# Kernel optimization log

Hardware: AMD Instinct MI355X
Metric: run time of the kernel (lower is better)

The kernel has to match this reference:

```python
import jax, jax.numpy as jnp
import numpy as np

N_NODES = 100_000
N_EDGES = 1_600_000
N_GRAPHS = 512
NF = 64        # n_node_feats
H1 = 128       # hidden width
H2 = 64        # dim_node_emb
DIM_OUT = 1
STEPS = 4      # set2set processing steps


def _lin(x, W, b):
    # torch Linear convention: y = x @ W.T + b, W: [out, in]
    return x @ W.T + b


def _gelu(x):
    return jax.nn.gelu(x, approximate=False)  # torch.nn.GELU default (erf)


def _lstm_cell(x, h, c, Wih, Whh, bih, bhh):
    g = x @ Wih.T + bih + h @ Whh.T + bhh
    i, f, gg, o = jnp.split(g, 4, axis=-1)  # torch gate order: i, f, g, o
    i, f, o = jax.nn.sigmoid(i), jax.nn.sigmoid(f), jax.nn.sigmoid(o)
    gg = jnp.tanh(gg)
    c = f * c + i * gg
    h = o * jnp.tanh(c)
    return h, c


def setup_inputs() -> dict:
    key = jax.random.key(0)
    ks = jax.random.split(key, 24)
    p = lambda k, shp: jax.random.normal(k, shp, dtype=jnp.float32) * 0.05
    inp = {
        "x": jax.random.normal(ks[0], (N_NODES, NF), dtype=jnp.float32),
        "edge_index": jax.random.randint(ks[1], (2, N_EDGES), 0, N_NODES, dtype=jnp.int32),
        "batch": jnp.sort(jax.random.randint(ks[2], (N_NODES,), 0, N_GRAPHS, dtype=jnp.int32)),
        "nfc_W": p(ks[3], (H1, NF)), "nfc_b": p(ks[4], (H1,)),
        "gc1_W": p(ks[5], (H1, H1)), "gc1_b": p(ks[6], (H1,)),
        "gc2_W": p(ks[7], (H2, H1)), "gc2_b": p(ks[8], (H2,)),
        "lstm0_Wih": p(ks[9], (4 * H2, 2 * H2)), "lstm0_Whh": p(ks[10], (4 * H2, H2)),
        "lstm0_bih": p(ks[11], (4 * H2,)), "lstm0_bhh": p(ks[12], (4 * H2,)),
        "lstm1_Wih": p(ks[13], (4 * H2, H2)), "lstm1_Whh": p(ks[14], (4 * H2, H2)),
        "lstm1_bih": p(ks[15], (4 * H2,)), "lstm1_bhh": p(ks[16], (4 * H2,)),
        "fc1_W": p(ks[17], (32, 2 * H2)), "fc1_b": p(ks[18], (32,)),
        "fc2_W": p(ks[19], (DIM_OUT, 32)), "fc2_b": p(ks[20], (DIM_OUT,)),
    }
    return inp


def _forward(x, edge_index, batch, nfc_W, nfc_b, gc1_W, gc1_b, gc2_W, gc2_b,
             lstm0_Wih, lstm0_Whh, lstm0_bih, lstm0_bhh,
             lstm1_Wih, lstm1_Whh, lstm1_bih, lstm1_bhh,
             fc1_W, fc1_b, fc2_W, fc2_b):
    src, dst = edge_index[0], edge_index[1]

    def gin_conv(h, W, b):
        # PyG GINConv, eps=0: lin((1+eps)*x + sum_{j in N(i)} x_j)
        agg = jax.ops.segment_sum(h[src], dst, num_segments=N_NODES)
        return _lin(h + agg, W, b)

    h = _gelu(_lin(x, nfc_W, nfc_b))
    h = _gelu(gin_conv(h, gc1_W, gc1_b))
    h = _gelu(gin_conv(h, gc2_W, gc2_b))
    # F.normalize(p=2, dim=1)
    h = h / jnp.maximum(jnp.linalg.norm(h, axis=1, keepdims=True), 1e-12)

    # Set2Set: 2-layer LSTM, 4 processing steps, scatter-softmax attention
    B = N_GRAPHS
    h0 = jnp.zeros((B, H2), jnp.float32); c0 = jnp.zeros((B, H2), jnp.float32)
    h1 = jnp.zeros((B, H2), jnp.float32); c1 = jnp.zeros((B, H2), jnp.float32)
    q_star = jnp.zeros((B, 2 * H2), jnp.float32)
    for _ in range(STEPS):
        h0, c0 = _lstm_cell(q_star, h0, c0, lstm0_Wih, lstm0_Whh, lstm0_bih, lstm0_bhh)
        h1, c1 = _lstm_cell(h0, h1, c1, lstm1_Wih, lstm1_Whh, lstm1_bih, lstm1_bhh)
        q = h1  # [B, H2]
        e = jnp.sum(h * q[batch], axis=-1, keepdims=True)  # [N, 1]
        m = jax.ops.segment_max(e, batch, num_segments=B)
        ex = jnp.exp(e - m[batch])
        s = jax.ops.segment_sum(ex, batch, num_segments=B)
        a = ex / (s[batch] + 1e-16)
        r = jax.ops.segment_sum(a * h, batch, num_segments=B)  # [B, H2]
        q_star = jnp.concatenate([q, r], axis=-1)

    z = _gelu(_lin(q_star, fc1_W, fc1_b))
    z = _lin(z, fc2_W, fc2_b)
    return z, h


def reference(x, edge_index, batch, nfc_W, nfc_b, gc1_W, gc1_b, gc2_W, gc2_b,
              lstm0_Wih, lstm0_Whh, lstm0_bih, lstm0_bhh,
              lstm1_Wih, lstm1_Whh, lstm1_bih, lstm1_bhh,
              fc1_W, fc1_b, fc2_W, fc2_b):
    return _forward(x, edge_index, batch, nfc_W, nfc_b, gc1_W, gc1_b, gc2_W, gc2_b,
                    lstm0_Wih, lstm0_Whh, lstm0_bih, lstm0_bhh,
                    lstm1_Wih, lstm1_Whh, lstm1_bih, lstm1_bhh,
                    fc1_W, fc1_b, fc2_W, fc2_b)
```

## Files before the change

kernel.cpp:

```cpp
#include <hip/hip_runtime.h>
#include <hip/hip_bf16.h>
#include <hip/hip_fp16.h>
#include <math.h>

constexpr int N  = 100000;
constexpr int E  = 1600000;
constexpr int NG = 512;
constexpr int NF = 64;
constexpr int H1 = 128;
constexpr int H2 = 64;

constexpr int BW   = 128;
constexpr int NB   = (N + BW - 1) / BW;
constexpr int CAP  = 2600;
constexpr int CHUNK = 4096;

constexpr int MAXN = 416;
constexpr int RST  = 68;

typedef __attribute__((ext_vector_type(8))) short short8;
typedef __attribute__((ext_vector_type(4))) float f32x4;

__device__ __forceinline__ float gelu_f(float x) {
    return 0.5f * x * (1.0f + erff(x * 0.70710678118654752f));
}
__device__ __forceinline__ float sigmoid_f(float x) {
    return 1.0f / (1.0f + expf(-x));
}
__device__ __forceinline__ float waveAllSum(float v) {
    #pragma unroll
    for (int m = 32; m; m >>= 1) v += __shfl_xor(v, m);
    return v;
}
__device__ __forceinline__ unsigned short f2bf(float x) {
    __hip_bfloat16 b = __float2bfloat16(x);
    return *reinterpret_cast<unsigned short*>(&b);
}
__device__ __forceinline__ float bf2f(unsigned short u) {
    return __uint_as_float(((unsigned int)u) << 16);
}
__device__ __forceinline__ float bf_lo(unsigned int u) { return __uint_as_float(u << 16); }
__device__ __forceinline__ float bf_hi(unsigned int u) { return __uint_as_float(u & 0xffff0000u); }

__device__ __forceinline__ void bfsplit(float v, unsigned short& hi, unsigned short& lo) {
    hi = f2bf(v);
    lo = f2bf(v - bf2f(hi));
}

__device__ __forceinline__ void pack8(float4 a, float4 b, short8& h8, short8& l8) {
    unsigned short h0,h1,h2,h3,h4,h5,h6,h7,l0,l1,l2,l3,l4,l5,l6,l7;
    bfsplit(a.x,h0,l0); bfsplit(a.y,h1,l1); bfsplit(a.z,h2,l2); bfsplit(a.w,h3,l3);
    bfsplit(b.x,h4,l4); bfsplit(b.y,h5,l5); bfsplit(b.z,h6,l6); bfsplit(b.w,h7,l7);
    union { uint4 u; short8 s; } th, tl;
    th.u = make_uint4((unsigned)h0|((unsigned)h1<<16),(unsigned)h2|((unsigned)h3<<16),
                      (unsigned)h4|((unsigned)h5<<16),(unsigned)h6|((unsigned)h7<<16));
    tl.u = make_uint4((unsigned)l0|((unsigned)l1<<16),(unsigned)l2|((unsigned)l3<<16),
                      (unsigned)l4|((unsigned)l5<<16),(unsigned)l6|((unsigned)l7<<16));
    h8 = th.s; l8 = tl.s;
}

__global__ __launch_bounds__(256) void setup_kernel(const int* __restrict__ batch,
                                                    const float* __restrict__ Wih0, const float* __restrict__ Whh0,
                                                    const float* __restrict__ bih0, const float* __restrict__ bhh0,
                                                    const float* __restrict__ Wih1, const float* __restrict__ Whh1,
                                                    const float* __restrict__ bih1, const float* __restrict__ bhh1,
                                                    const float* __restrict__ gc1W, const float* __restrict__ gc2W,
                                                    const float* __restrict__ nfcW,
                                                    float* __restrict__ WT0, float* __restrict__ WT1,
                                                    float* __restrict__ b0, float* __restrict__ b1,
                                                    unsigned short* __restrict__ W1F, unsigned short* __restrict__ W2F,
                                                    unsigned short* __restrict__ W0F,
                                                    int* __restrict__ bcursor, int* __restrict__ gstart) {
    int i = blockIdx.x * 256 + threadIdx.x;
    if (i < 192 * 256) {
        int k = i >> 8, j = i & 255;
        WT0[i] = (k < 128) ? Wih0[j * 128 + k] : Whh0[j * 64 + (k - 128)];
    }
    if (i < 128 * 256) {
        int k = i >> 8, j = i & 255;
        WT1[i] = (k < 64) ? Wih1[j * 64 + k] : Whh1[j * 64 + (k - 64)];
    }
    if (i < 16384) {
        int f = i >> 9, r = i & 511, l = r >> 3, j = r & 7;
        int c = f >> 3, ct = f & 7;
        int o = ct * 16 + (l & 15), k = c * 32 + (l >> 4) * 8 + j;
        unsigned short hi, lo;
        bfsplit(gc1W[o * 128 + k], hi, lo);
        W1F[f * 1024 + r] = hi;
        W1F[f * 1024 + 512 + r] = lo;
    }
    if (i < 8192) {
        int f = i >> 9, r = i & 511, l = r >> 3, j = r & 7;
        int c2 = f >> 2, ct2 = f & 3;
        int o = ct2 * 16 + (l & 15), k = c2 * 32 + (l >> 4) * 8 + j;
        unsigned short hi, lo;
        bfsplit(gc2W[o * 128 + k], hi, lo);
        W2F[f * 1024 + r] = hi;
        W2F[f * 1024 + 512 + r] = lo;
    }
    if (i < 8192) {
        int f = i >> 9, r = i & 511, l = r >> 3, j = r & 7;
        int c = f >> 3, ct = f & 7;
        int o = ct * 16 + (l & 15), k = c * 32 + (l >> 4) * 8 + j;
        unsigned short hi, lo;
        bfsplit(nfcW[o * 64 + k], hi, lo);
        W0F[f * 1024 + r] = hi;
        W0F[f * 1024 + 512 + r] = lo;
    }
    if (i < 256) { b0[i] = bih0[i] + bhh0[i]; b1[i] = bih1[i] + bhh1[i]; }
    if (i < NB) bcursor[i] = i * CAP;
    if (i <= NG) {
        if (i == NG) gstart[NG] = N;
        else {
            int lo = 0, hi = N;
            while (lo < hi) {
                int mid = (lo + hi) >> 1;
                if (batch[mid] < i) lo = mid + 1; else hi = mid;
            }
            gstart[i] = lo;
        }
    }
}

__global__ __launch_bounds__(256) void bin_scatter_kernel(const int* __restrict__ ei,
                                                          int* __restrict__ bcursor,
                                                          int* __restrict__ pairs) {
    __shared__ int hist[NB];
    __shared__ int start_s[NB];
    __shared__ int lcur[NB];
    int tid = threadIdx.x;
    int e0 = blockIdx.x * CHUNK;
    for (int b = tid; b < NB; b += 256) hist[b] = 0;
    __syncthreads();
    #pragma unroll 4
    for (int k = 0; k < CHUNK / 256; ++k) {
        int e = e0 + k * 256 + tid;
        if (e < E) atomicAdd(&hist[ei[E + e] >> 7], 1);
    }
    __syncthreads();
    for (int b = tid; b < NB; b += 256) {
        if (hist[b]) start_s[b] = atomicAdd(&bcursor[b], hist[b]);
        lcur[b] = 0;
    }
    __syncthreads();
    #pragma unroll 4
    for (int k = 0; k < CHUNK / 256; ++k) {
        int e = e0 + k * 256 + tid;
        if (e < E) {
            int d = ei[E + e];
            int s = ei[e];
            int b = d >> 7;
            int pos = start_s[b] + atomicAdd(&lcur[b], 1);
            if (pos < (b + 1) * CAP) pairs[pos] = (s << 7) | (d & 127);
        }
    }
}

__global__ __launch_bounds__(256) void csr_bucket_kernel(const int* __restrict__ pairs,
                                                         const int* __restrict__ bcursor,
                                                         int* __restrict__ srcs,
                                                         int2* __restrict__ nrange) {
    __shared__ int cnt_l[BW];
    __shared__ int cur_l[BW];
    __shared__ int wt[2];
    int b = blockIdx.x;
    int tid = threadIdx.x;
    int base = b * CAP;
    int cnt = bcursor[b] - base;
    if (cnt > CAP) cnt = CAP;
    if (tid < BW) cnt_l[tid] = 0;
    __syncthreads();
    for (int i = tid; i < cnt; i += 256) {
        atomicAdd(&cnt_l[pairs[base + i] & 127], 1);
    }
    __syncthreads();
    if (tid < BW) {
        int v = cnt_l[tid];
        int lane = tid & 63, w = tid >> 6;
        int incl = v;
        #pragma unroll
        for (int off = 1; off < 64; off <<= 1) {
            int t = __shfl_up(incl, off);
            if (lane >= off) incl += t;
        }
        if (lane == 63) wt[w] = incl;
        __syncthreads();
        int excl = (w ? wt[0] : 0) + incl - v;
        int node = b * BW + tid;
        if (node < N) nrange[node] = make_int2(base + excl, base + excl + v);
        cur_l[tid] = excl;
    } else {
        __syncthreads();
    }
    __syncthreads();
    for (int i = tid; i < cnt; i += 256) {
        int p = pairs[base + i];
        int pos = atomicAdd(&cur_l[p & 127], 1);
        srcs[base + pos] = p >> 7;
    }
}

__global__ __launch_bounds__(512, 2) void lin1_kernel(const float* __restrict__ x,
                                                      const uint4* __restrict__ W0F,
                                                      const float* __restrict__ bias,
                                                      unsigned short* __restrict__ out_bf, int nrows) {
    constexpr int EPS = 136;
    __shared__ __align__(16) uint4 w0lds[2048];
    __shared__ __align__(16) unsigned short eps[8][16 * EPS];
    union U8 { uint4 u; short8 s; };
    int tid = threadIdx.x, w = tid >> 6, lane = tid & 63;
    int m15 = lane & 15, quad = lane >> 4;
    int rowbase = blockIdx.x * 128 + w * 16;
    int r0 = rowbase + m15; if (r0 >= nrows) r0 = nrows - 1;

    #pragma unroll
    for (int i = 0; i < 4; ++i) w0lds[i * 512 + tid] = W0F[i * 512 + tid];
    __syncthreads();

    f32x4 acc[8];
    #pragma unroll
    for (int ct = 0; ct < 8; ++ct) acc[ct] = (f32x4)0.f;

    float4 p0[2][2];
    #pragma unroll
    for (int c = 0; c < 2; ++c) {
        p0[c][0] = *(const float4*)&x[(size_t)r0 * 64 + c * 32 + quad * 8];
        p0[c][1] = *(const float4*)&x[(size_t)r0 * 64 + c * 32 + quad * 8 + 4];
    }

    #pragma unroll
    for (int c = 0; c < 2; ++c) {
        short8 ah0, al0;
        pack8(p0[c][0], p0[c][1], ah0, al0);
        #pragma unroll
        for (int ct = 0; ct < 8; ++ct) {
            U8 th, tl;
            th.u = w0lds[(c * 8 + ct) * 128 + lane];
            tl.u = w0lds[(c * 8 + ct) * 128 + 64 + lane];
            short8 bh = th.s, bl = tl.s;
            acc[ct] = __builtin_amdgcn_mfma_f32_16x16x32_bf16(ah0, bh, acc[ct], 0, 0, 0);
            acc[ct] = __builtin_amdgcn_mfma_f32_16x16x32_bf16(ah0, bl, acc[ct], 0, 0, 0);
            acc[ct] = __builtin_amdgcn_mfma_f32_16x16x32_bf16(al0, bh, acc[ct], 0, 0, 0);
        }
    }

    unsigned short* ep = eps[w];
    #pragma unroll
    for (int ct = 0; ct < 8; ++ct) {
        float bc = bias[ct * 16 + m15];
        #pragma unroll
        for (int r = 0; r < 4; ++r) {
            int node = quad * 4 + r;
            ep[node * EPS + ct * 16 + m15] = f2bf(gelu_f(acc[ct][r] + bc));
        }
    }
    asm volatile("s_waitcnt lgkmcnt(0)" ::: "memory");
    #pragma unroll
    for (int it = 0; it < 4; ++it) {
        int idx = it * 64 + lane;
        int rowl = idx >> 4, off = (idx & 15) * 8;
        int grow = rowbase + rowl;
        if (grow < nrows)
            *(uint4*)(out_bf + (size_t)grow * 128 + off) = *(const uint4*)&ep[rowl * EPS + off];
    }
}

__global__ __launch_bounds__(256) void agg_kernel(const uint4* __restrict__ h4,
                                                  const int2* __restrict__ nrange,
                                                  const int* __restrict__ srcs,
                                                  uint4* __restrict__ utab) {
    int wave = threadIdx.x >> 6, lane = threadIdx.x & 63;
    int qw = lane >> 4, ql = lane & 15;
    int n = blockIdx.x * 4 + wave;
    if (n >= N) return;
    int2 rng = nrange[n];
    int s0 = rng.x, deg = rng.y - rng.x;
    int m1 = deg < 64 ? deg : 64;
    int pre = (lane < m1) ? srcs[s0 + lane] : 0;
    float a0 = 0.f, a1 = 0.f, a2 = 0.f, a3 = 0.f, a4 = 0.f, a5 = 0.f, a6 = 0.f, a7 = 0.f;
    auto addu = [&](uint4 u) {
        a0 += bf_lo(u.x); a1 += bf_hi(u.x); a2 += bf_lo(u.y); a3 += bf_hi(u.y);
        a4 += bf_lo(u.z); a5 += bf_hi(u.z); a6 += bf_lo(u.w); a7 += bf_hi(u.w);
    };
    int t = 0;
    for (; t + 16 <= m1; t += 16) {
        int i0 = __shfl(pre, t + qw);
        int i1 = __shfl(pre, t + 4 + qw);
        int i2 = __shfl(pre, t + 8 + qw);
        int i3 = __shfl(pre, t + 12 + qw);
        uint4 u0 = h4[(size_t)i0 * 16 + ql];
        uint4 u1 = h4[(size_t)i1 * 16 + ql];
        uint4 u2 = h4[(size_t)i2 * 16 + ql];
        uint4 u3 = h4[(size_t)i3 * 16 + ql];
        addu(u0); addu(u1); addu(u2); addu(u3);
    }
    for (; t < m1; t += 4) {
        int idx = t + qw;
        int s = __shfl(pre, idx < m1 ? idx : 0);
        if (idx < m1) addu(h4[(size_t)s * 16 + ql]);
    }
    for (int j = 64 + qw; j < deg; j += 4) addu(h4[(size_t)srcs[s0 + j] * 16 + ql]);
    a0 += __shfl_down(a0, 32); a1 += __shfl_down(a1, 32);
    a2 += __shfl_down(a2, 32); a3 += __shfl_down(a3, 32);
    a4 += __shfl_down(a4, 32); a5 += __shfl_down(a5, 32);
    a6 += __shfl_down(a6, 32); a7 += __shfl_down(a7, 32);
    a0 += __shfl_down(a0, 16); a1 += __shfl_down(a1, 16);
    a2 += __shfl_down(a2, 16); a3 += __shfl_down(a3, 16);
    a4 += __shfl_down(a4, 16); a5 += __shfl_down(a5, 16);
    a6 += __shfl_down(a6, 16); a7 += __shfl_down(a7, 16);
    if (qw == 0) {
        addu(h4[(size_t)n * 16 + ql]);
        unsigned short h0, h1, h2, h3, h4_, h5, h6, h7;
        unsigned short l0, l1, l2, l3, l4, l5, l6, l7;
        bfsplit(a0, h0, l0); bfsplit(a1, h1, l1);
        bfsplit(a2, h2, l2); bfsplit(a3, h3, l3);
        bfsplit(a4, h4_, l4); bfsplit(a5, h5, l5);
        bfsplit(a6, h6, l6); bfsplit(a7, h7, l7);
        uint4 o0, o1;
        o0.x = (unsigned)h0 | ((unsigned)h1 << 16);
        o0.y = (unsigned)h2 | ((unsigned)h3 << 16);
        o0.z = (unsigned)l0 | ((unsigned)l1 << 16);
        o0.w = (unsigned)l2 | ((unsigned)l3 << 16);
        o1.x = (unsigned)h4_ | ((unsigned)h5 << 16);
        o1.y = (unsigned)h6 | ((unsigned)h7 << 16);
        o1.z = (unsigned)l4 | ((unsigned)l5 << 16);
        o1.w = (unsigned)l6 | ((unsigned)l7 << 16);
        utab[(size_t)n * 32 + 2 * ql]     = o0;
        utab[(size_t)n * 32 + 2 * ql + 1] = o1;
    }
}

__global__ __launch_bounds__(512, 2) void lin2_fused_kernel(const uint4* __restrict__ in4,
                                                            const uint4* __restrict__ W1F,
                                                            const float* __restrict__ b1,
                                                            const uint4* __restrict__ W2F,
                                                            unsigned short* __restrict__ y2,
                                                            int nrows) {
    constexpr int AST2 = 40;
    __shared__ __align__(16) uint4 wlds[6144];
    __shared__ __align__(16) unsigned short relds[8 * 1280];
    union U8 { uint4 u; short8 s; };
    int tid = threadIdx.x, w = tid >> 6, lane = tid & 63;
    int m15 = lane & 15, quad = lane >> 4;
    unsigned short* myL = relds + w * 1280;
    int rowbase = blockIdx.x * 128 + w * 16;
    int r0 = rowbase + m15; if (r0 >= nrows) r0 = nrows - 1;
    const uint4* a0p = in4 + (size_t)r0 * 32 + quad * 2;

    #pragma unroll
    for (int i = 0; i < 12; ++i) {
        int idx = i * 512 + tid;
        wlds[idx] = (idx < 4096) ? W1F[idx] : W2F[idx - 4096];
    }

    uint4 a[8];
    #pragma unroll
    for (int c = 0; c < 4; ++c) { a[2 * c] = a0p[c * 8]; a[2 * c + 1] = a0p[c * 8 + 1]; }

    float bc[8];
    #pragma unroll
    for (int ct = 0; ct < 8; ++ct) bc[ct] = b1[ct * 16 + m15];

    __syncthreads();
    const uint4* W1L = wlds;
    const uint4* W2L = wlds + 4096;

    f32x4 acc[8];
    #pragma unroll
    for (int ct = 0; ct < 8; ++ct) acc[ct] = (f32x4)0.f;

    #pragma unroll
    for (int c = 0; c < 4; ++c) {
        U8 t;
        uint4 u00 = a[2 * c], u01 = a[2 * c + 1];
        t.u = make_uint4(u00.x, u00.y, u01.x, u01.y); short8 ah0 = t.s;
        t.u = make_uint4(u00.z, u00.w, u01.z, u01.w); short8 al0 = t.s;
        #pragma unroll
        for (int ct = 0; ct < 8; ++ct) {
            U8 th, tl;
            th.u = W1L[(c * 8 + ct) * 128 + lane];
            tl.u = W1L[(c * 8 + ct) * 128 + 64 + lane];
            short8 bh = th.s, bl = tl.s;
            acc[ct] = __builtin_amdgcn_mfma_f32_16x16x32_bf16(ah0, bh, acc[ct], 0, 0, 0);
            acc[ct] = __builtin_amdgcn_mfma_f32_16x16x32_bf16(ah0, bl, acc[ct], 0, 0, 0);
            acc[ct] = __builtin_amdgcn_mfma_f32_16x16x32_bf16(al0, bh, acc[ct], 0, 0, 0);
        }
    }

    #pragma unroll
    for (int ct = 0; ct < 8; ++ct)
        #pragma unroll
        for (int r = 0; r < 4; ++r)
            acc[ct][r] = gelu_f(acc[ct][r] + bc[ct]);

    unsigned short* Ahi2 = myL;
    unsigned short* Alo2 = myL + 16 * AST2;
    f32x4 acc2[4];
    #pragma unroll
    for (int ct = 0; ct < 4; ++ct) acc2[ct] = (f32x4)0.f;

    #pragma unroll
    for (int c2 = 0; c2 < 4; ++c2) {
        #pragma unroll
        for (int cc = 0; cc < 2; ++cc) {
            int ct = c2 * 2 + cc;
            #pragma unroll
            for (int r = 0; r < 4; ++r) {
                int node = quad * 4 + r;
                unsigned short hi, lo;
                bfsplit(acc[ct][r], hi, lo);
                Ahi2[node * AST2 + cc * 16 + m15] = hi;
                Alo2[node * AST2 + cc * 16 + m15] = lo;
            }
        }
        asm volatile("s_waitcnt lgkmcnt(0)" ::: "memory");
        short8 ah0 = *(const short8*)&Ahi2[m15 * AST2 + quad * 8];
        short8 al0 = *(const short8*)&Alo2[m15 * AST2 + quad * 8];
        #pragma unroll
        for (int ct2 = 0; ct2 < 4; ++ct2) {
            U8 th, tl;
            th.u = W2L[(c2 * 4 + ct2) * 128 + lane];
            tl.u = W2L[(c2 * 4 + ct2) * 128 + 64 + lane];
            short8 bh = th.s, bl = tl.s;
            acc2[ct2] = __builtin_amdgcn_mfma_f32_16x16x32_bf16(ah0, bh, acc2[ct2], 0, 0, 0);
            acc2[ct2] = __builtin_amdgcn_mfma_f32_16x16x32_bf16(ah0, bl, acc2[ct2], 0, 0, 0);
            acc2[ct2] = __builtin_amdgcn_mfma_f32_16x16x32_bf16(al0, bh, acc2[ct2], 0, 0, 0);
        }
    }

    unsigned short* ep = myL;
    #pragma unroll
    for (int ct2 = 0; ct2 < 4; ++ct2)
        #pragma unroll
        for (int r = 0; r < 4; ++r) {
            int node = quad * 4 + r;
            __half hv = __float2half(acc2[ct2][r]);
            ep[node * 72 + ct2 * 16 + m15] = *reinterpret_cast<unsigned short*>(&hv);
        }
    asm volatile("s_waitcnt lgkmcnt(0)" ::: "memory");
    #pragma unroll
    for (int it = 0; it < 2; ++it) {
        int idx = it * 64 + lane;
        int rowl = idx >> 3, off = (idx & 7) * 8;
        int grow = rowbase + rowl;
        if (grow < nrows)
            *(uint4*)(y2 + (size_t)grow * 64 + off) = *(const uint4*)&ep[rowl * 72 + off];
    }
}

__global__ __launch_bounds__(256) void agg2_norm_kernel(const uint2* __restrict__ y2,
                                                        const int2* __restrict__ nrange,
                                                        const int* __restrict__ srcs,
                                                        const float* __restrict__ b2,
                                                        float* __restrict__ hn) {
    int wave = threadIdx.x >> 6, lane = threadIdx.x & 63;
    int qw = lane >> 4, ql = lane & 15;
    int n = blockIdx.x * 4 + wave;
    if (n >= N) return;
    int2 rng = nrange[n];
    int s0 = rng.x, deg = rng.y - rng.x;
    int m1 = deg < 64 ? deg : 64;
    int pre = (lane < m1) ? srcs[s0 + lane] : 0;
    float a0 = 0.f, a1 = 0.f, a2 = 0.f, a3 = 0.f;
    auto addu = [&](uint2 u) {
        float2 f01 = __half22float2(*reinterpret_cast<__half2*>(&u.x));
        float2 f23 = __half22float2(*reinterpret_cast<__half2*>(&u.y));
        a0 += f01.x; a1 += f01.y; a2 += f23.x; a3 += f23.y;
    };
    int t = 0;
    for (; t + 16 <= m1; t += 16) {
        int i0 = __shfl(pre, t + qw);
        int i1 = __shfl(pre, t + 4 + qw);
        int i2 = __shfl(pre, t + 8 + qw);
        int i3 = __shfl(pre, t + 12 + qw);
        uint2 u0 = y2[(size_t)i0 * 16 + ql];
        uint2 u1 = y2[(size_t)i1 * 16 + ql];
        uint2 u2 = y2[(size_t)i2 * 16 + ql];
        uint2 u3 = y2[(size_t)i3 * 16 + ql];
        addu(u0); addu(u1); addu(u2); addu(u3);
    }
    for (; t < m1; t += 4) {
        int idx = t + qw;
        int s = __shfl(pre, idx < m1 ? idx : 0);
        if (idx < m1) addu(y2[(size_t)s * 16 + ql]);
    }
    for (int j = 64 + qw; j < deg; j += 4) addu(y2[(size_t)srcs[s0 + j] * 16 + ql]);
    a0 += __shfl_down(a0, 32); a1 += __shfl_down(a1, 32);
    a2 += __shfl_down(a2, 32); a3 += __shfl_down(a3, 32);
    a0 += __shfl_down(a0, 16); a1 += __shfl_down(a1, 16);
    a2 += __shfl_down(a2, 16); a3 += __shfl_down(a3, 16);
    if (qw == 0) {
        addu(y2[(size_t)n * 16 + ql]);
        float4 bv = *(const float4*)&b2[ql * 4];
        float v0 = gelu_f(a0 + bv.x), v1 = gelu_f(a1 + bv.y);
        float v2 = gelu_f(a2 + bv.z), v3 = gelu_f(a3 + bv.w);
        float ss = v0 * v0 + v1 * v1 + v2 * v2 + v3 * v3;
        #pragma unroll
        for (int mm = 1; mm < 16; mm <<= 1) ss += __shfl_xor(ss, mm);
        float d = fmaxf(sqrtf(ss), 1e-12f);
        *(float4*)&hn[(size_t)n * 64 + ql * 4] = make_float4(v0 / d, v1 / d, v2 / d, v3 / d);
    }
}

__global__ __launch_bounds__(256) void set2set_kernel(const float* __restrict__ hn,
                                                      const int* __restrict__ gstart,
                                                      const float* __restrict__ WT0, const float* __restrict__ b0,
                                                      const float* __restrict__ WT1, const float* __restrict__ b1,
                                                      float* __restrict__ qstar_out) {
    __shared__ __align__(16) unsigned short hL[MAXN * RST];
    __shared__ float av[MAXN];
    __shared__ __align__(16) float xc0[192];
    __shared__ __align__(16) float xc1[128];
    __shared__ __align__(16) float gates[256];
    __shared__ float c0v[H2], c1v[H2];
    __shared__ float red[4];
    __shared__ float rp[4][H2];
    __shared__ float sp[4];

    int g = blockIdx.x;
    int tid = threadIdx.x, w = tid >> 6, lane = tid & 63;
    int s0 = gstart[g], s1 = gstart[g + 1];
    int cnt = s1 - s0;
    int cL = cnt < MAXN ? cnt : MAXN;
    const float* hq = xc1 + 64;

    for (int idx = tid; idx < cL * 16; idx += 256) {
        int n = idx >> 4, p4 = idx & 15;
        float4 v = *(const float4*)&hn[(size_t)(s0 + n) * 64 + p4 * 4];
        uint2 u;
        u.x = (unsigned int)f2bf(v.x) | ((unsigned int)f2bf(v.y) << 16);
        u.y = (unsigned int)f2bf(v.z) | ((unsigned int)f2bf(v.w) << 16);
        *(uint2*)&hL[n * RST + p4 * 4] = u;
    }
    if (tid < 192) xc0[tid] = 0.f;
    if (tid < 128) xc1[tid] = 0.f;
    if (tid < H2) { c0v[tid] = 0.f; c1v[tid] = 0.f; }
    float b0v = b0[tid], b1v = b1[tid];
    __syncthreads();

    for (int step = 0; step < 4; ++step) {
        {
            float a0 = 0.f, a1 = 0.f, a2 = 0.f, a3 = 0.f;
            #pragma unroll 8
            for (int k = 0; k < 192; k += 4) {
                a0 += xc0[k]     * WT0[(k)     * 256 + tid];
                a1 += xc0[k + 1] * WT0[(k + 1) * 256 + tid];
                a2 += xc0[k + 2] * WT0[(k + 2) * 256 + tid];
                a3 += xc0[k + 3] * WT0[(k + 3) * 256 + tid];
            }
            gates[tid] = (a0 + a1) + (a2 + a3) + b0v;
        }
        __syncthreads();
        if (tid < H2) {
            float ii = sigmoid_f(gates[tid]), ff = sigmoid_f(gates[H2 + tid]);
            float gg = tanhf(gates[2 * H2 + tid]), oo = sigmoid_f(gates[3 * H2 + tid]);
            float c = ff * c0v[tid] + ii * gg;
            float h = oo * tanhf(c);
            c0v[tid] = c; xc0[128 + tid] = h; xc1[tid] = h;
        }
        __syncthreads();
        {
            float a0 = 0.f, a1 = 0.f, a2 = 0.f, a3 = 0.f;
            #pragma unroll 8
            for (int k = 0; k < 128; k += 4) {
                a0 += xc1[k]     * WT1[(k)     * 256 + tid];
                a1 += xc1[k + 1] * WT1[(k + 1) * 256 + tid];
                a2 += xc1[k + 2] * WT1[(k + 2) * 256 + tid];
                a3 += xc1[k + 3] * WT1[(k + 3) * 256 + tid];
            }
            gates[tid] = (a0 + a1) + (a2 + a3) + b1v;
        }
        __syncthreads();
        if (tid < H2) {
            float ii = sigmoid_f(gates[tid]), ff = sigmoid_f(gates[H2 + tid]);
            float gg = tanhf(gates[2 * H2 + tid]), oo = sigmoid_f(gates[3 * H2 + tid]);
            float c = ff * c1v[tid] + ii * gg;
            float h = oo * tanhf(c);
            c1v[tid] = c; xc1[64 + tid] = h;
        }
        __syncthreads();

        float lm = -INFINITY;
        for (int i = tid; i < cnt; i += 256) {
            float e = 0.f;
            if (i < MAXN) {
                const uint2* row = (const uint2*)&hL[i * RST];
                #pragma unroll
                for (int p4 = 0; p4 < 16; ++p4) {
                    uint2 u = row[p4];
                    e += bf_lo(u.x) * hq[p4 * 4 + 0];
                    e += bf_hi(u.x) * hq[p4 * 4 + 1];
                    e += bf_lo(u.y) * hq[p4 * 4 + 2];
                    e += bf_hi(u.y) * hq[p4 * 4 + 3];
                }
                av[i] = e;
            } else {
                for (int f = 0; f < 64; ++f) e += hn[(size_t)(s0 + i) * 64 + f] * hq[f];
            }
            lm = fmaxf(lm, e);
        }
        #pragma unroll
        for (int mm = 32; mm; mm >>= 1) lm = fmaxf(lm, __shfl_xor(lm, mm));
        if (lane == 0) red[w] = lm;
        __syncthreads();
        float m = fmaxf(fmaxf(red[0], red[1]), fmaxf(red[2], red[3]));

        float ps = 0.f;
        for (int i = tid; i < cnt; i += 256) {
            float e;
            if (i < MAXN) e = av[i];
            else {
                e = 0.f;
                for (int f = 0; f < 64; ++f) e += hn[(size_t)(s0 + i) * 64 + f] * hq[f];
            }
            float p = expf(e - m);
            ps += p;
            if (i < MAXN) av[i] = p;
        }
        ps = waveAllSum(ps);
        if (lane == 0) sp[w] = ps;
        __syncthreads();
        float s = sp[0] + sp[1] + sp[2] + sp[3];

        float racc = 0.f;
        for (int i = w; i < cL; i += 4) {
            unsigned short hv = hL[i * RST + lane];
            racc += av[i] * bf2f(hv);
        }
        float qf = hq[lane];
        for (int n = MAXN + w; n < cnt; n += 4) {
            float v = hn[(size_t)(s0 + n) * 64 + lane];
            float e = waveAllSum(v * qf);
            float p = expf(e - m);
            racc += p * v;
        }
        rp[w][lane] = racc;
        __syncthreads();
        if (tid < H2) {
            float r = 0.f;
            if (cnt > 0) {
                r = (rp[0][tid] + rp[1][tid] + rp[2][tid] + rp[3][tid]) / (s + 1e-16f);
            }
            xc0[tid] = xc1[64 + tid];
            xc0[H2 + tid] = r;
        }
        __syncthreads();
    }
    if (tid < 2 * H2) qstar_out[g * 2 * H2 + tid] = xc0[tid];
}

__global__ __launch_bounds__(256) void fcout_kernel(const float* __restrict__ q_star,
                                                    const float* __restrict__ W1, const float* __restrict__ b1,
                                                    const float* __restrict__ W2, const float* __restrict__ b2,
                                                    float* __restrict__ z) {
    __shared__ float W1l[32 * 128];
    __shared__ float b1l[32], W2l[32];
    int tid = threadIdx.x;
    for (int i = tid; i < 32 * 128; i += 256) W1l[i] = W1[i];
    if (tid < 32) { b1l[tid] = b1[tid]; W2l[tid] = W2[tid]; }
    __syncthreads();
    int g = blockIdx.x * 256 + tid;
    float acc[32];
    #pragma unroll
    for (int j = 0; j < 32; ++j) acc[j] = b1l[j];
    for (int k = 0; k < 128; ++k) {
        float qv = q_star[g * 128 + k];
        #pragma unroll
        for (int j = 0; j < 32; ++j) acc[j] += qv * W1l[j * 128 + k];
    }
    float zv = b2[0];
    #pragma unroll
    for (int j = 0; j < 32; ++j) zv += gelu_f(acc[j]) * W2l[j];
    z[g] = zv;
}

extern "C" void kernel_launch(void* const* d_in, const int* in_sizes, int n_in,
                              void* d_out, int out_size, void* d_ws, size_t ws_size,
                              hipStream_t stream) {
    const float* x       = (const float*)d_in[0];
    const int*   ei      = (const int*)d_in[1];
    const int*   batch   = (const int*)d_in[2];
    const float* nfc_W   = (const float*)d_in[3];
    const float* nfc_b   = (const float*)d_in[4];
    const float* gc1_W   = (const float*)d_in[5];
    const float* gc1_b   = (const float*)d_in[6];
    const float* gc2_W   = (const float*)d_in[7];
    const float* gc2_b   = (const float*)d_in[8];
    const float* l0_Wih  = (const float*)d_in[9];
    const float* l0_Whh  = (const float*)d_in[10];
    const float* l0_bih  = (const float*)d_in[11];
    const float* l0_bhh  = (const float*)d_in[12];
    const float* l1_Wih  = (const float*)d_in[13];
    const float* l1_Whh  = (const float*)d_in[14];
    const float* l1_bih  = (const float*)d_in[15];
    const float* l1_bhh  = (const float*)d_in[16];
    const float* fc1_W   = (const float*)d_in[17];
    const float* fc1_b   = (const float*)d_in[18];
    const float* fc2_W   = (const float*)d_in[19];
    const float* fc2_b   = (const float*)d_in[20];

    float* out = (float*)d_out;
    float* hn_out = out + NG;

    char* p = (char*)d_ws;
    auto take = [&](size_t bytes) {
        char* r = p;
        p += (bytes + 255) & ~size_t(255);
        return r;
    };
    float*          sbuf  = (float*)take((size_t)N * H1 * 4);
    unsigned short* hbbuf = (unsigned short*)take((size_t)N * H1 * 2);
    int*   srcs   = (int*)take((size_t)NB * CAP * 4);
    int2*  nrange = (int2*)take((size_t)N * 8);
    int*   bcursor= (int*)take((size_t)NB * 4);
    int*   gstart = (int*)take((size_t)(NG + 1) * 4);
    float* qstar  = (float*)take((size_t)NG * 2 * H2 * 4);
    float* WT0    = (float*)take((size_t)192 * 256 * 4);
    float* WT1    = (float*)take((size_t)128 * 256 * 4);
    float* b0     = (float*)take((size_t)256 * 4);
    float* b1     = (float*)take((size_t)256 * 4);
    unsigned short* W1F = (unsigned short*)take((size_t)32 * 1024 * 2);
    unsigned short* W2F = (unsigned short*)take((size_t)16 * 1024 * 2);
    unsigned short* W0F = (unsigned short*)take((size_t)16 * 1024 * 2);

    int* pairs = (int*)sbuf;

    setup_kernel<<<192, 256, 0, stream>>>(batch, l0_Wih, l0_Whh, l0_bih, l0_bhh,
                                          l1_Wih, l1_Whh, l1_bih, l1_bhh,
                                          gc1_W, gc2_W, nfc_W,
                                          WT0, WT1, b0, b1, W1F, W2F, W0F, bcursor, gstart);

    bin_scatter_kernel<<<(E + CHUNK - 1) / CHUNK, 256, 0, stream>>>(ei, bcursor, pairs);
    csr_bucket_kernel<<<NB, 256, 0, stream>>>(pairs, bcursor, srcs, nrange);

    int linGrid = (N + 127) / 128;
    lin1_kernel<<<linGrid, 512, 0, stream>>>(x, (const uint4*)W0F, nfc_b, hbbuf, N);
    agg_kernel<<<(N + 3) / 4, 256, 0, stream>>>((const uint4*)hbbuf, nrange, srcs, (uint4*)sbuf);
    lin2_fused_kernel<<<linGrid, 512, 0, stream>>>((const uint4*)sbuf, (const uint4*)W1F, gc1_b,
                                                   (const uint4*)W2F, hbbuf, N);
    agg2_norm_kernel<<<(N + 3) / 4, 256, 0, stream>>>((const uint2*)hbbuf, nrange, srcs,
                                                      gc2_b, hn_out);

    set2set_kernel<<<NG, 256, 0, stream>>>(hn_out, gstart, WT0, b0, WT1, b1, qstar);

    fcout_kernel<<<2, 256, 0, stream>>>(qstar, fc1_W, fc1_b, fc2_W, fc2_b, out);
}
```

Measured before the change: 408.7 us.

## Split first aggregation into feature halves and fuse output MLP into set2set

The first neighbor aggregation now runs as two launches, each gathering only half of the 128 bf16 features per node, with 8 edges processed per wave iteration instead of 4. This shrinks each pass's gather working set so more of it stays in cache, at the cost of reading the index lists twice and adding a launch. Separately, the final fc1/GELU/fc2 head is folded into the end of the set2set kernel using a transposed fc1 weight copy in shared memory. That removes the q_star buffer round-trip and one launch, but every graph block now reloads the fc1 weights.

```diff
diff --git a/kernel.cpp b/kernel.cpp
--- a/kernel.cpp
+++ b/kernel.cpp
@@ -265,18 +265,20 @@
     }
 }
 
-__global__ __launch_bounds__(256) void agg_kernel(const uint4* __restrict__ h4,
-                                                  const int2* __restrict__ nrange,
-                                                  const int* __restrict__ srcs,
-                                                  uint4* __restrict__ utab) {
+__global__ __launch_bounds__(256) void agg_half_kernel(const uint4* __restrict__ h4,
+                                                       const int2* __restrict__ nrange,
+                                                       const int* __restrict__ srcs,
+                                                       uint4* __restrict__ utab,
+                                                       int half) {
     int wave = threadIdx.x >> 6, lane = threadIdx.x & 63;
-    int qw = lane >> 4, ql = lane & 15;
+    int ew = lane >> 3, el = lane & 7;
     int n = blockIdx.x * 4 + wave;
     if (n >= N) return;
     int2 rng = nrange[n];
     int s0 = rng.x, deg = rng.y - rng.x;
     int m1 = deg < 64 ? deg : 64;
     int pre = (lane < m1) ? srcs[s0 + lane] : 0;
+    int hofs = half * 8 + el;
     float a0 = 0.f, a1 = 0.f, a2 = 0.f, a3 = 0.f, a4 = 0.f, a5 = 0.f, a6 = 0.f, a7 = 0.f;
     auto addu = [&](uint4 u) {
         a0 += bf_lo(u.x); a1 += bf_hi(u.x); a2 += bf_lo(u.y); a3 += bf_hi(u.y);
@@ -284,22 +286,18 @@
     };
     int t = 0;
     for (; t + 16 <= m1; t += 16) {
-        int i0 = __shfl(pre, t + qw);
-        int i1 = __shfl(pre, t + 4 + qw);
-        int i2 = __shfl(pre, t + 8 + qw);
-        int i3 = __shfl(pre, t + 12 + qw);
-        uint4 u0 = h4[(size_t)i0 * 16 + ql];
-        uint4 u1 = h4[(size_t)i1 * 16 + ql];
-        uint4 u2 = h4[(size_t)i2 * 16 + ql];
-        uint4 u3 = h4[(size_t)i3 * 16 + ql];
-        addu(u0); addu(u1); addu(u2); addu(u3);
-    }
-    for (; t < m1; t += 4) {
-        int idx = t + qw;
+        int i0 = __shfl(pre, t + ew);
+        int i1 = __shfl(pre, t + 8 + ew);
+        uint4 u0 = h4[(size_t)i0 * 16 + hofs];
+        uint4 u1 = h4[(size_t)i1 * 16 + hofs];
+        addu(u0); addu(u1);
+    }
+    for (; t < m1; t += 8) {
+        int idx = t + ew;
         int s = __shfl(pre, idx < m1 ? idx : 0);
-        if (idx < m1) addu(h4[(size_t)s * 16 + ql]);
-    }
-    for (int j = 64 + qw; j < deg; j += 4) addu(h4[(size_t)srcs[s0 + j] * 16 + ql]);
+        if (idx < m1) addu(h4[(size_t)s * 16 + hofs]);
+    }
+    for (int j = 64 + ew; j < deg; j += 8) addu(h4[(size_t)srcs[s0 + j] * 16 + hofs]);
     a0 += __shfl_down(a0, 32); a1 += __shfl_down(a1, 32);
     a2 += __shfl_down(a2, 32); a3 += __shfl_down(a3, 32);
     a4 += __shfl_down(a4, 32); a5 += __shfl_down(a5, 32);
@@ -308,8 +306,12 @@
     a2 += __shfl_down(a2, 16); a3 += __shfl_down(a3, 16);
     a4 += __shfl_down(a4, 16); a5 += __shfl_down(a5, 16);
     a6 += __shfl_down(a6, 16); a7 += __shfl_down(a7, 16);
-    if (qw == 0) {
-        addu(h4[(size_t)n * 16 + ql]);
+    a0 += __shfl_down(a0, 8);  a1 += __shfl_down(a1, 8);
+    a2 += __shfl_down(a2, 8);  a3 += __shfl_down(a3, 8);
+    a4 += __shfl_down(a4, 8);  a5 += __shfl_down(a5, 8);
+    a6 += __shfl_down(a6, 8);  a7 += __shfl_down(a7, 8);
+    if (ew == 0) {
+        addu(h4[(size_t)n * 16 + hofs]);
         unsigned short h0, h1, h2, h3, h4_, h5, h6, h7;
         unsigned short l0, l1, l2, l3, l4, l5, l6, l7;
         bfsplit(a0, h0, l0); bfsplit(a1, h1, l1);
@@ -325,8 +327,9 @@
         o1.y = (unsigned)h6 | ((unsigned)h7 << 16);
         o1.z = (unsigned)l4 | ((unsigned)l5 << 16);
         o1.w = (unsigned)l6 | ((unsigned)l7 << 16);
-        utab[(size_t)n * 32 + 2 * ql]     = o0;
-        utab[(size_t)n * 32 + 2 * ql + 1] = o1;
+        int g0 = half * 16 + 2 * el;
+        utab[(size_t)n * 32 + g0]     = o0;
+        utab[(size_t)n * 32 + g0 + 1] = o1;
     }
 }
 
@@ -506,7 +509,9 @@
                                                       const int* __restrict__ gstart,
                                                       const float* __restrict__ WT0, const float* __restrict__ b0,
                                                       const float* __restrict__ WT1, const float* __restrict__ b1,
-                                                      float* __restrict__ qstar_out) {
+                                                      const float* __restrict__ fc1W, const float* __restrict__ fc1b,
+                                                      const float* __restrict__ fc2W, const float* __restrict__ fc2b,
+                                                      float* __restrict__ zout) {
     __shared__ __align__(16) unsigned short hL[MAXN * RST];
     __shared__ float av[MAXN];
     __shared__ __align__(16) float xc0[192];
@@ -516,6 +521,7 @@
     __shared__ float red[4];
     __shared__ float rp[4][H2];
     __shared__ float sp[4];
+    __shared__ float fcWT[128 * 32];
 
     int g = blockIdx.x;
     int tid = threadIdx.x, w = tid >> 6, lane = tid & 63;
@@ -531,6 +537,10 @@
         u.x = (unsigned int)f2bf(v.x) | ((unsigned int)f2bf(v.y) << 16);
         u.y = (unsigned int)f2bf(v.z) | ((unsigned int)f2bf(v.w) << 16);
         *(uint2*)&hL[n * RST + p4 * 4] = u;
+    }
+    for (int i = tid; i < 4096; i += 256) {
+        int j = i >> 7, k = i & 127;
+        fcWT[k * 32 + j] = fc1W[i];
     }
     if (tid < 192) xc0[tid] = 0.f;
     if (tid < 128) xc1[tid] = 0.f;
@@ -646,32 +656,18 @@
         }
         __syncthreads();
     }
-    if (tid < 2 * H2) qstar_out[g * 2 * H2 + tid] = xc0[tid];
-}
-
-__global__ __launch_bounds__(256) void fcout_kernel(const float* __restrict__ q_star,
-                                                    const float* __restrict__ W1, const float* __restrict__ b1,
-                                                    const float* __restrict__ W2, const float* __restrict__ b2,
-                                                    float* __restrict__ z) {
-    __shared__ float W1l[32 * 128];
-    __shared__ float b1l[32], W2l[32];
-    int tid = threadIdx.x;
-    for (int i = tid; i < 32 * 128; i += 256) W1l[i] = W1[i];
-    if (tid < 32) { b1l[tid] = b1[tid]; W2l[tid] = W2[tid]; }
-    __syncthreads();
-    int g = blockIdx.x * 256 + tid;
-    float acc[32];
-    #pragma unroll
-    for (int j = 0; j < 32; ++j) acc[j] = b1l[j];
-    for (int k = 0; k < 128; ++k) {
-        float qv = q_star[g * 128 + k];
-        #pragma unroll
-        for (int j = 0; j < 32; ++j) acc[j] += qv * W1l[j * 128 + k];
-    }
-    float zv = b2[0];
-    #pragma unroll
-    for (int j = 0; j < 32; ++j) zv += gelu_f(acc[j]) * W2l[j];
-    z[g] = zv;
+
+    if (w == 0) {
+        float zv = 0.f;
+        if (lane < 32) {
+            float a = fc1b[lane];
+            #pragma unroll 8
+            for (int k = 0; k < 128; ++k) a += xc0[k] * fcWT[k * 32 + lane];
+            zv = gelu_f(a) * fc2W[lane];
+        }
+        zv = waveAllSum(zv);
+        if (lane == 0) zout[g] = zv + fc2b[0];
+    }
 }
 
 extern "C" void kernel_launch(void* const* d_in, const int* in_sizes, int n_in,
@@ -714,7 +710,6 @@
     int2*  nrange = (int2*)take((size_t)N * 8);
     int*   bcursor= (int*)take((size_t)NB * 4);
     int*   gstart = (int*)take((size_t)(NG + 1) * 4);
-    float* qstar  = (float*)take((size_t)NG * 2 * H2 * 4);
     float* WT0    = (float*)take((size_t)192 * 256 * 4);
     float* WT1    = (float*)take((size_t)128 * 256 * 4);
     float* b0     = (float*)take((size_t)256 * 4);
@@ -735,13 +730,15 @@
 
     int linGrid = (N + 127) / 128;
     lin1_kernel<<<linGrid, 512, 0, stream>>>(x, (const uint4*)W0F, nfc_b, hbbuf, N);
-    agg_kernel<<<(N + 3) / 4, 256, 0, stream>>>((const uint4*)hbbuf, nrange, srcs, (uint4*)sbuf);
+    agg_half_kernel<<<(N + 3) / 4, 256, 0, stream>>>((const uint4*)hbbuf, nrange, srcs,
+                                                     (uint4*)sbuf, 0);
+    agg_half_kernel<<<(N + 3) / 4, 256, 0, stream>>>((const uint4*)hbbuf, nrange, srcs,
+                                                     (uint4*)sbuf, 1);
     lin2_fused_kernel<<<linGrid, 512, 0, stream>>>((const uint4*)sbuf, (const uint4*)W1F, gc1_b,
                                                    (const uint4*)W2F, hbbuf, N);
     agg2_norm_kernel<<<(N + 3) / 4, 256, 0, stream>>>((const uint2*)hbbuf, nrange, srcs,
                                                       gc2_b, hn_out);
 
-    set2set_kernel<<<NG, 256, 0, stream>>>(hn_out, gstart, WT0, b0, WT1, b1, qstar);
-
-    fcout_kernel<<<2, 256, 0, stream>>>(qstar, fc1_W, fc1_b, fc2_W, fc2_b, out);
-}
+    set2set_kernel<<<NG, 256, 0, stream>>>(hn_out, gstart, WT0, b0, WT1, b1,
+                                           fc1_W, fc1_b, fc2_W, fc2_b, out);
+}
```

Result: slower. 423.1 us (+3.5%).
